# Optimization experiments

Hardware: AMD Instinct MI355X
Metric: run time of the kernel (lower is better)

The kernel has to match this reference:

```python
import jax, jax.numpy as jnp
import numpy as np

HEADS = 20          # 1280 / 64 head_dim, standard SD UNet attention
LORA_SCALE = 1.0    # lora_scale init arg


def setup_inputs() -> dict:
    key = jax.random.key(0)
    ks = jax.random.split(key, 16)
    def w(k, shape, s=0.02):
        return jax.random.normal(k, shape, dtype=jnp.float32) * s
    H, C, R = 1280, 768, 64  # hidden_size, cross_attention_dim, lora_rank
    return {
        "hidden_states": jax.random.normal(ks[0], (16, 4096, H), dtype=jnp.float32),
        "encoder_hidden_states": jax.random.normal(ks[1], (16, 77, C), dtype=jnp.float32),
        # base attention projections (diffusers: q/k/v no bias, to_out has bias)
        "Wq": w(ks[2], (H, H)), "Wk": w(ks[3], (C, H)), "Wv": w(ks[4], (C, H)),
        "Wo": w(ks[5], (H, H)), "bo": jnp.zeros((H,), dtype=jnp.float32),
        # LoRA adapters (down: in->rank, up: rank->out, no bias)
        "q_down": w(ks[6], (H, R)), "q_up": w(ks[7], (R, H)),
        "k_down": w(ks[8], (C, R)), "k_up": w(ks[9], (R, H)),
        "v_down": w(ks[10], (C, R)), "v_up": w(ks[11], (R, H)),
        "o_down": w(ks[12], (H, R)), "o_up": w(ks[13], (R, H)),
    }


def reference(hidden_states, encoder_hidden_states, Wq, Wk, Wv, Wo, bo,
              q_down, q_up, k_down, k_up, v_down, v_up, o_down, o_up):
    b, sq, _ = hidden_states.shape
    # base projections + LoRA low-rank corrections
    q = hidden_states @ Wq + LORA_SCALE * ((hidden_states @ q_down) @ q_up)
    k = encoder_hidden_states @ Wk + LORA_SCALE * ((encoder_hidden_states @ k_down) @ k_up)
    v = encoder_hidden_states @ Wv + LORA_SCALE * ((encoder_hidden_states @ v_down) @ v_up)

    d = q.shape[-1] // HEADS
    def split_heads(x):  # [b, s, h*d] -> [b, h, s, d]
        return x.reshape(x.shape[0], x.shape[1], HEADS, d).transpose(0, 2, 1, 3)
    qh, kh, vh = split_heads(q), split_heads(k), split_heads(v)

    # scaled dot-product attention (no mask, non-causal, dropout=0)
    scale = 1.0 / np.sqrt(d).astype(np.float32)
    scores = jnp.einsum('bhqd,bhkd->bhqk', qh, kh) * scale
    probs = jax.nn.softmax(scores, axis=-1)
    attn_out = jnp.einsum('bhqk,bhkd->bhqd', probs, vh)
    attn_out = attn_out.transpose(0, 2, 1, 3).reshape(b, sq, HEADS * d)

    # output projection + LoRA on W_O
    out = attn_out @ Wo + bo + LORA_SCALE * ((attn_out @ o_down) @ o_up)
    return out
```

## Files before the change

### kernel.cpp

```cpp
#include <hip/hip_runtime.h>
#include <hip/hip_bf16.h>
#include <stdint.h>

typedef unsigned short u16;
typedef __attribute__((ext_vector_type(8))) short short8;
typedef __attribute__((ext_vector_type(4))) float f32x4;

__device__ __forceinline__ u16 f2bf(float f) {
  union { float f; unsigned u; } v; v.f = f;
  unsigned r = v.u + 0x7fffu + ((v.u >> 16) & 1u);
  return (u16)(r >> 16);
}

__device__ __forceinline__ void g2lds16(const u16* g, u16* l) {
  __builtin_amdgcn_global_load_lds(
      (const __attribute__((address_space(1))) uint32_t*)g,
      (__attribute__((address_space(3))) uint32_t*)l, 16, 0, 0);
}

#define BAR()   asm volatile("s_barrier" ::: "memory")
#define LGKM0() asm volatile("s_waitcnt lgkmcnt(0)" ::: "memory")
#define VM8()   asm volatile("s_waitcnt vmcnt(8)" ::: "memory")
#define VM0()   asm volatile("s_waitcnt vmcnt(0)" ::: "memory")
#define PRIO1() __builtin_amdgcn_s_setprio(1)
#define PRIO0() __builtin_amdgcn_s_setprio(0)

#define QSCALE 0.18033688f

__global__ __launch_bounds__(256) void k_convert(const float* __restrict__ in,
                                                 u16* __restrict__ out, int n8) {
  int i = blockIdx.x * 256 + threadIdx.x;
  if (i >= n8) return;
  const float4* p = (const float4*)(in + (size_t)i * 8);
  float4 a = p[0], b = p[1];
  short8 o;
  o[0] = (short)f2bf(a.x); o[1] = (short)f2bf(a.y);
  o[2] = (short)f2bf(a.z); o[3] = (short)f2bf(a.w);
  o[4] = (short)f2bf(b.x); o[5] = (short)f2bf(b.y);
  o[6] = (short)f2bf(b.z); o[7] = (short)f2bf(b.w);
  *(short8*)(out + (size_t)i * 8) = o;
}

__global__ __launch_bounds__(256) void k_prep(
    const float* __restrict__ ehs, u16* __restrict__ ehs_b,
    const float* __restrict__ Wq, const float* __restrict__ qd, const float* __restrict__ qu, u16* __restrict__ wq_t,
    const float* __restrict__ Wk, const float* __restrict__ kd, const float* __restrict__ ku, u16* __restrict__ wk_t,
    const float* __restrict__ Wv, const float* __restrict__ vd, const float* __restrict__ vu, u16* __restrict__ wv_t,
    const float* __restrict__ Wo, const float* __restrict__ od, const float* __restrict__ ou, u16* __restrict__ wo_t) {
  __shared__ float dn[64][65];
  __shared__ float up[64][17];
  int bid = blockIdx.x;

  if (bid < 480) {
    int i = bid * 256 + threadIdx.x;
    short8 o;
    if (i < 118272) {
      const float4* p = (const float4*)(ehs + (size_t)i * 8);
      float4 a = p[0], b = p[1];
      o[0] = (short)f2bf(a.x); o[1] = (short)f2bf(a.y);
      o[2] = (short)f2bf(a.z); o[3] = (short)f2bf(a.w);
      o[4] = (short)f2bf(b.x); o[5] = (short)f2bf(b.y);
      o[6] = (short)f2bf(b.z); o[7] = (short)f2bf(b.w);
    } else {
#pragma unroll
      for (int e = 0; e < 8; ++e) o[e] = 0;
    }
    *(short8*)(ehs_b + (size_t)i * 8) = o;
    return;
  }
  bid -= 480;
  const float *W, *dng, *upg; u16* Wt; int K, bx, by;
  if (bid < 1600)      { W = Wq; dng = qd; upg = qu; Wt = wq_t; K = 1280; bx = bid % 20; by = bid / 20; }
  else if (bid < 2560) { bid -= 1600; W = Wk; dng = kd; upg = ku; Wt = wk_t; K = 768;  bx = bid % 12; by = bid / 12; }
  else if (bid < 3520) { bid -= 2560; W = Wv; dng = vd; upg = vu; Wt = wv_t; K = 768;  bx = bid % 12; by = bid / 12; }
  else                 { bid -= 3520; W = Wo; dng = od; upg = ou; Wt = wo_t; K = 1280; bx = bid % 20; by = bid / 20; }
  const int N = 1280;
  const int k0 = bx * 64, n0 = by * 16;
  const int kc = threadIdx.x & 63, ty = threadIdx.x >> 6;
  for (int c = threadIdx.x; c < 4096; c += 256)
    dn[c >> 6][c & 63] = dng[(size_t)(k0 + (c >> 6)) * 64 + (c & 63)];
  for (int c = threadIdx.x; c < 1024; c += 256)
    up[c >> 4][c & 15] = upg[(size_t)(c >> 4) * N + n0 + (c & 15)];
  __syncthreads();
  float acc[4];
#pragma unroll
  for (int e = 0; e < 4; ++e)
    acc[e] = W[(size_t)(k0 + kc) * N + n0 + ty * 4 + e];
#pragma unroll 16
  for (int r = 0; r < 64; ++r) {
    float d = dn[kc][r];
#pragma unroll
    for (int e = 0; e < 4; ++e) acc[e] += d * up[r][ty * 4 + e];
  }
#pragma unroll
  for (int e = 0; e < 4; ++e)
    Wt[(size_t)(n0 + ty * 4 + e) * K + k0 + kc] = f2bf(acc[e]);
}

__global__ __launch_bounds__(256) void k_gemmKV(const u16* __restrict__ A,
                                                const u16* __restrict__ BtK,
                                                const u16* __restrict__ BtV,
                                                u16* __restrict__ CK,
                                                u16* __restrict__ CV) {
  constexpr int N = 1280, K = 768;
  const u16* Bt = blockIdx.z ? BtV : BtK;
  u16* Cout = blockIdx.z ? CV : CK;
  __shared__ __align__(16) u16 As[128 * 32];
  __shared__ __align__(16) u16 Bs[128 * 32];
  const int tid = threadIdx.x, lane = tid & 63, w = tid >> 6;
  const int n0 = blockIdx.x * 128, m0 = blockIdx.y * 128;
  const int wm = (w >> 1) * 64, wn = (w & 1) * 64;

  f32x4 acc[4][4];
  f32x4 zf = {0.f, 0.f, 0.f, 0.f};
#pragma unroll
  for (int i = 0; i < 4; ++i)
#pragma unroll
    for (int j = 0; j < 4; ++j) acc[i][j] = zf;

  const int c0 = w, c1 = w + 4;
  const int rA0 = c0 * 16 + (lane >> 2), rA1 = c1 * 16 + (lane >> 2);
  const int kp = (lane & 3) * 8;
  const u16* gA0 = A + (size_t)(m0 + rA0) * K + kp;
  const u16* gA1 = A + (size_t)(m0 + rA1) * K + kp;
  const u16* gB0 = Bt + (size_t)(n0 + rA0) * K + kp;
  const u16* gB1 = Bt + (size_t)(n0 + rA1) * K + kp;
  u16* lA0 = As + c0 * 512;  u16* lA1 = As + c1 * 512;
  u16* lB0 = Bs + c0 * 512;  u16* lB1 = Bs + c1 * 512;

  const int fr = lane & 15, kg = (lane >> 4) * 8;

  for (int k0 = 0; k0 < K; k0 += 32) {
    g2lds16(gA0 + k0, lA0);
    g2lds16(gA1 + k0, lA1);
    g2lds16(gB0 + k0, lB0);
    g2lds16(gB1 + k0, lB1);
    __syncthreads();
    short8 af[4], bf[4];
#pragma unroll
    for (int i = 0; i < 4; ++i)
      af[i] = *(const short8*)(As + (wm + i * 16 + fr) * 32 + kg);
#pragma unroll
    for (int j = 0; j < 4; ++j)
      bf[j] = *(const short8*)(Bs + (wn + j * 16 + fr) * 32 + kg);
#pragma unroll
    for (int i = 0; i < 4; ++i)
#pragma unroll
      for (int j = 0; j < 4; ++j)
        acc[i][j] = __builtin_amdgcn_mfma_f32_16x16x32_bf16(af[i], bf[j], acc[i][j], 0, 0, 0);
    __syncthreads();
  }

  const int rb = (lane >> 4) * 4;
#pragma unroll
  for (int i = 0; i < 4; ++i)
#pragma unroll
    for (int j = 0; j < 4; ++j) {
      int col = n0 + wn + j * 16 + fr;
#pragma unroll
      for (int r = 0; r < 4; ++r) {
        int row = m0 + wm + i * 16 + rb + r;
        Cout[(size_t)row * N + col] = f2bf(acc[i][j][r]);
      }
    }
}

#define GEMM256_TILE_RD()                                                      \
  constexpr int K = 1280;                                                      \
  constexpr int N = 1280;                                                      \
  __shared__ __align__(16) u16 lds[2][2][2][128 * 64];                         \
  const int lane = threadIdx.x & 63, w = threadIdx.x >> 6;                     \
  const int bid = blockIdx.x;                                                  \
  const int tile = (bid & 7) * 160 + (bid >> 3);                               \
  const int n0 = (tile % 5) * 256, m0 = (tile / 5) * 256;                      \
  const int l0 = w * 2;                                                        \
  const int fr = lane & 15;                                                    \
  const int q16b = (lane >> 4) * 16;                                           \
  const int xr = (fr & 7) << 4;                                                \
  const int cT0 = ((0 + q16b) ^ xr) >> 1;                                      \
  const int cT1 = ((64 + q16b) ^ xr) >> 1;                                     \
  const int ha = w >> 2;                                                       \
  const int hb = (w & 3) >> 1;                                                 \
  const int rB0 = (w & 1) * 64;

#define LOAD_AF(P, IB)                                                         \
  do {                                                                         \
    _Pragma("unroll") for (int ii = 0; ii < 4; ++ii) {                         \
      const u16* rp = &lds[P][0][ha][(((IB) + ii) * 16 + fr) * 64];            \
      af[ii][0] = *(const short8*)(rp + cT0);                                  \
      af[ii][1] = *(const short8*)(rp + cT1);                                  \
    }                                                                          \
  } while (0)

#define LOAD_BF(P, JB)                                                         \
  do {                                                                         \
    _Pragma("unroll") for (int jj = 0; jj < 2; ++jj) {                         \
      const u16* rp = &lds[P][1][hb][(rB0 + ((JB) + jj) * 16 + fr) * 64];      \
      bf[(JB) + jj][0] = *(const short8*)(rp + cT0);                           \
      bf[(JB) + jj][1] = *(const short8*)(rp + cT1);                           \
    }                                                                          \
  } while (0)

#define MFMA_Q(IO, JB)                                                         \
  do {                                                                         \
    _Pragma("unroll") for (int t = 0; t < 2; ++t)                              \
        _Pragma("unroll") for (int ii = 0; ii < 4; ++ii)                       \
            _Pragma("unroll") for (int jj = 0; jj < 2; ++jj)                   \
                acc[(IO) + ii][(JB) + jj] =                                    \
        __builtin_amdgcn_mfma_f32_16x16x32_bf16(                               \
            af[ii][t], bf[(JB) + jj][t], acc[(IO) + ii][(JB) + jj], 0, 0, 0);  \
  } while (0)

#define ACC_ZERO()                                                             \
  do {                                                                         \
    f32x4 zf = {0.f, 0.f, 0.f, 0.f};                                           \
    _Pragma("unroll") for (int i = 0; i < 8; ++i)                              \
        _Pragma("unroll") for (int j = 0; j < 4; ++j) acc[i][j] = zf;          \
  } while (0)

template <int OUT_MODE>
__global__ __launch_bounds__(512, 2) void k_gemm256f(const u16* __restrict__ A,
                                                     const u16* __restrict__ Bt,
                                                     void* __restrict__ Cout,
                                                     const float* __restrict__ bias) {
  GEMM256_TILE_RD();
  const u16* gsrc[8];
#pragma unroll
  for (int s = 0; s < 8; ++s) {
    const int side = s >> 2, h = (s >> 1) & 1, l = s & 1;
    const int o = (l0 + l) * 1024 + lane * 16;
    const int row = o >> 7;
    const int scol = (o & 127) ^ ((row & 7) << 4);
    const u16* base = side ? (Bt + (size_t)(n0 + h * 128 + row) * K)
                           : (A + (size_t)(m0 + h * 128 + row) * K);
    gsrc[s] = base + (scol >> 1);
  }

#define STAGE(P, KT)                                                           \
  do {                                                                         \
    _Pragma("unroll") for (int s = 0; s < 8; ++s) {                            \
      const int side = s >> 2, h = (s >> 1) & 1, l = s & 1;                    \
      g2lds16(gsrc[s] + (KT) * 64, &lds[P][side][h][(l0 + l) * 512]);          \
    }                                                                          \
  } while (0)

  short8 af[4][2], bf[4][2];
  f32x4 acc[8][4];
  ACC_ZERO();

  STAGE(0, 0);
  STAGE(1, 1);
  VM8();
  BAR();

  for (int t = 0; t < 20; ++t) {
    const int P = t & 1;
    LOAD_AF(P, 0);
    LOAD_BF(P, 0);
    LOAD_BF(P, 2);
    MFMA_Q(0, 0);
    MFMA_Q(0, 2);
    LOAD_AF(P, 4);
    MFMA_Q(4, 2);
    LGKM0();
    BAR();
    if (t < 18) STAGE(P, t + 2);
    PRIO1(); MFMA_Q(4, 0); PRIO0();
    if (t < 18) { VM8(); } else { VM0(); }
    BAR();
  }
#undef STAGE

  const int rb = (lane >> 4) * 4;
  const int orow = m0 + (w >> 2) * 128;
  const int ocol = n0 + (w & 3) * 64;
  if (OUT_MODE == 1) {
    float* C = (float*)Cout;
#pragma unroll
    for (int i = 0; i < 8; ++i)
#pragma unroll
      for (int j = 0; j < 4; ++j) {
        const int col = ocol + j * 16 + fr;
        const float bj = bias[col];
#pragma unroll
        for (int r = 0; r < 4; ++r)
          C[(size_t)(orow + i * 16 + rb + r) * N + col] = acc[i][j][r] + bj;
      }
  } else {
    u16* C = (u16*)Cout;
#pragma unroll
    for (int i = 0; i < 8; ++i)
#pragma unroll
      for (int j = 0; j < 4; ++j) {
        const int col = ocol + j * 16 + fr;
#pragma unroll
        for (int r = 0; r < 4; ++r)
          C[(size_t)(orow + i * 16 + rb + r) * N + col] = f2bf(acc[i][j][r] * QSCALE);
      }
  }
}

__global__ __launch_bounds__(256) void k_attn(u16* __restrict__ Q,
                                              const u16* __restrict__ Kb,
                                              const u16* __restrict__ Vb) {
  const int mt = blockIdx.x, h = blockIdx.y, b = blockIdx.z;
  const int tid = threadIdx.x, lane = tid & 63, w = tid >> 6;
  const int m0 = b * 4096 + mt * 128;
  const int ccol = h * 64;

  __shared__ __align__(16) u16 Qs[128 * 64];
  __shared__ __align__(16) u16 Kl[80 * 72];
  __shared__ __align__(16) u16 Vt[64 * 104];
  __shared__ __align__(16) u16 Pl[128 * 104];

#pragma unroll
  for (int c = 0; c < 4; ++c) {
    const int o = (c * 4 + w) * 1024 + lane * 16;
    const int row = o >> 7;
    const int scol = (o & 127) ^ ((row & 7) << 4);
    g2lds16(Q + (size_t)(m0 + row) * 1280 + ccol + (scol >> 1),
            Qs + (size_t)(c * 4 + w) * 512);
  }

  {
    short8 zz;
#pragma unroll
    for (int e = 0; e < 8; ++e) zz[e] = 0;
    if (tid < 27) ((short8*)Kl)[693 + tid] = zz;
    { const int prow = tid >> 1, pc0 = 80 + (tid & 1) * 8;
      *(short8*)(Pl + prow * 104 + pc0) = zz; }
    for (int c = tid; c < 2048; c += 256)
      Vt[(c >> 5) * 104 + 64 + (c & 31)] = 0;
  }
  for (int c = tid; c < 616; c += 256) {
    int s = c >> 3, d0 = (c & 7) * 8;
    short8 v = *(const short8*)(Kb + (size_t)(b * 77 + s) * 1280 + ccol + d0);
    *(short8*)(Kl + s * 72 + d0) = v;
  }
  for (int c = tid; c < 616; c += 256) {
    int s = c >> 3, d0 = (c & 7) * 8;
    short8 v = *(const short8*)(Vb + (size_t)(b * 77 + s) * 1280 + ccol + d0);
#pragma unroll
    for (int e = 0; e < 8; ++e) Vt[(d0 + e) * 104 + s] = (u16)v[e];
  }
  __syncthreads();

  const int cb = lane & 15;
  const int kq = lane >> 4;
  const int kgu = kq * 8;

  short8 qf[2][2];
#pragma unroll
  for (int i = 0; i < 2; ++i)
#pragma unroll
    for (int t2 = 0; t2 < 2; ++t2) {
      const int r_ = w * 32 + i * 16 + cb;
      const int bc = (t2 * 64 + kq * 16) ^ ((r_ & 7) << 4);
      qf[i][t2] = *(const short8*)(Qs + r_ * 64 + (bc >> 1));
    }

  f32x4 sc[2][5];
  {
    f32x4 zf = {0.f, 0.f, 0.f, 0.f};
#pragma unroll
    for (int i = 0; i < 2; ++i)
#pragma unroll
      for (int j = 0; j < 5; ++j) sc[i][j] = zf;
  }
#pragma unroll
  for (int t2 = 0; t2 < 2; ++t2) {
    short8 kf[5];
#pragma unroll
    for (int j = 0; j < 5; ++j)
      kf[j] = *(const short8*)(Kl + (j * 16 + cb) * 72 + t2 * 32 + kgu);
#pragma unroll
    for (int i = 0; i < 2; ++i)
#pragma unroll
      for (int j = 0; j < 5; ++j)
        sc[i][j] = __builtin_amdgcn_mfma_f32_16x16x32_bf16(qf[i][t2], kf[j], sc[i][j], 0, 0, 0);
  }

  float inv[2][4];
#pragma unroll
  for (int i = 0; i < 2; ++i) {
#pragma unroll
    for (int r = 0; r < 4; ++r) {
      float sum = 0.f;
#pragma unroll
      for (int j = 0; j < 4; ++j) {
        float pv = exp2f(sc[i][j][r]);
        sc[i][j][r] = pv;
        sum += pv;
      }
      {
        float pv = (cb < 13) ? exp2f(sc[i][4][r]) : 0.f;
        sc[i][4][r] = pv;
        sum += pv;
      }
#pragma unroll
      for (int mk = 8; mk >= 1; mk >>= 1) sum += __shfl_xor(sum, mk, 64);
      inv[i][r] = 1.f / sum;
    }
  }

  {
    const int rbase = kq * 4;
#pragma unroll
    for (int i = 0; i < 2; ++i)
#pragma unroll
      for (int j = 0; j < 5; ++j)
#pragma unroll
        for (int r = 0; r < 4; ++r)
          Pl[(w * 32 + i * 16 + rbase + r) * 104 + j * 16 + cb] = f2bf(sc[i][j][r]);
  }
  __syncthreads();

  f32x4 o[2][4];
  {
    f32x4 zf = {0.f, 0.f, 0.f, 0.f};
#pragma unroll
    for (int i = 0; i < 2; ++i)
#pragma unroll
      for (int n = 0; n < 4; ++n) o[i][n] = zf;
  }
#pragma unroll
  for (int t2 = 0; t2 < 3; ++t2) {
    short8 pf[2], vf[4];
#pragma unroll
    for (int i = 0; i < 2; ++i)
      pf[i] = *(const short8*)(Pl + (w * 32 + i * 16 + cb) * 104 + t2 * 32 + kgu);
#pragma unroll
    for (int n = 0; n < 4; ++n)
      vf[n] = *(const short8*)(Vt + (n * 16 + cb) * 104 + t2 * 32 + kgu);
#pragma unroll
    for (int i = 0; i < 2; ++i)
#pragma unroll
      for (int n = 0; n < 4; ++n)
        o[i][n] = __builtin_amdgcn_mfma_f32_16x16x32_bf16(pf[i], vf[n], o[i][n], 0, 0, 0);
  }

  {
    const int rbase = kq * 4;
#pragma unroll
    for (int i = 0; i < 2; ++i)
#pragma unroll
      for (int n = 0; n < 4; ++n)
#pragma unroll
        for (int r = 0; r < 4; ++r)
          Pl[(w * 32 + i * 16 + rbase + r) * 104 + n * 16 + cb] =
              f2bf(o[i][n][r] * inv[i][r]);
  }
  __syncthreads();

#pragma unroll
  for (int c2 = 0; c2 < 4; ++c2) {
    const int o2 = (c2 * 256 + tid) * 16;
    const int row = o2 >> 7, bc = (o2 & 127) >> 1;
    short8 v = *(const short8*)(Pl + row * 104 + bc);
    *(short8*)(Q + (size_t)(m0 + row) * 1280 + ccol + bc) = v;
  }
}

extern "C" void kernel_launch(void* const* d_in, const int* in_sizes, int n_in,
                              void* d_out, int out_size, void* d_ws, size_t ws_size,
                              hipStream_t stream) {
  (void)in_sizes; (void)n_in; (void)out_size; (void)ws_size;
  const float* hs  = (const float*)d_in[0];
  const float* ehs = (const float*)d_in[1];
  const float* Wq  = (const float*)d_in[2];
  const float* Wk  = (const float*)d_in[3];
  const float* Wv  = (const float*)d_in[4];
  const float* Wo  = (const float*)d_in[5];
  const float* bo  = (const float*)d_in[6];
  const float* qd  = (const float*)d_in[7];
  const float* qu  = (const float*)d_in[8];
  const float* kd  = (const float*)d_in[9];
  const float* ku  = (const float*)d_in[10];
  const float* vd  = (const float*)d_in[11];
  const float* vu  = (const float*)d_in[12];
  const float* od  = (const float*)d_in[13];
  const float* ou  = (const float*)d_in[14];

  char* p = (char*)d_ws;
  u16* q_buf = (u16*)p;  p += (size_t)65536 * 1280 * 2;
  u16* wq_t  = (u16*)p;  p += (size_t)1280 * 1280 * 2;
  u16* wo_t  = (u16*)p;  p += (size_t)1280 * 1280 * 2;
  u16* wk_t  = (u16*)p;  p += (size_t)1280 * 768 * 2;
  u16* wv_t  = (u16*)p;  p += (size_t)1280 * 768 * 2;
  u16* ehs_b = (u16*)p;  p += (size_t)1280 * 768 * 2;
  u16* k_buf = (u16*)p;  p += (size_t)1280 * 1280 * 2;
  u16* v_buf = (u16*)p;  p += (size_t)1280 * 1280 * 2;
  u16* hs_b  = (u16*)d_out;

  k_convert<<<40960, 256, 0, stream>>>(hs, hs_b, 10485760);
  k_prep<<<5600, 256, 0, stream>>>(ehs, ehs_b,
                                   Wq, qd, qu, wq_t,
                                   Wk, kd, ku, wk_t,
                                   Wv, vd, vu, wv_t,
                                   Wo, od, ou, wo_t);

  k_gemm256f<2><<<1280, 512, 0, stream>>>(hs_b, wq_t, q_buf, nullptr);
  k_gemmKV<<<dim3(10, 10, 2), 256, 0, stream>>>(ehs_b, wk_t, wv_t, k_buf, v_buf);

  k_attn<<<dim3(32, 20, 16), 256, 0, stream>>>(q_buf, k_buf, v_buf);

  k_gemm256f<1><<<1280, 512, 0, stream>>>(q_buf, wo_t, d_out, bo);
}
```

Measured before the change: 746.7 us.

## Load B operand directly from global to registers in Q-projection GEMM

Adds a GEMM variant that stages only the A tile through LDS and loads the weight (B) fragments straight from global memory into registers each k-step. LDS use per block is halved and B no longer makes an LDS round trip, while the waitcnt thresholds are adjusted to match. Only the Q projection uses the new kernel. The direct global loads of B are less coalesced and sit in the critical path right before the MFMAs, so latency may be exposed.

```diff
diff --git a/kernel.cpp b/kernel.cpp
--- a/kernel.cpp
+++ b/kernel.cpp
@@ -21,6 +21,7 @@
 #define BAR()   asm volatile("s_barrier" ::: "memory")
 #define LGKM0() asm volatile("s_waitcnt lgkmcnt(0)" ::: "memory")
 #define VM8()   asm volatile("s_waitcnt vmcnt(8)" ::: "memory")
+#define VM4()   asm volatile("s_waitcnt vmcnt(4)" ::: "memory")
 #define VM0()   asm volatile("s_waitcnt vmcnt(0)" ::: "memory")
 #define PRIO1() __builtin_amdgcn_s_setprio(1)
 #define PRIO0() __builtin_amdgcn_s_setprio(0)
@@ -165,10 +166,9 @@
     }
 }
 
-#define GEMM256_TILE_RD()                                                      \
+#define GEMM256_COMMON()                                                       \
   constexpr int K = 1280;                                                      \
   constexpr int N = 1280;                                                      \
-  __shared__ __align__(16) u16 lds[2][2][2][128 * 64];                         \
   const int lane = threadIdx.x & 63, w = threadIdx.x >> 6;                     \
   const int bid = blockIdx.x;                                                  \
   const int tile = (bid & 7) * 160 + (bid >> 3);                               \
@@ -183,24 +183,6 @@
   const int hb = (w & 3) >> 1;                                                 \
   const int rB0 = (w & 1) * 64;
 
-#define LOAD_AF(P, IB)                                                         \
-  do {                                                                         \
-    _Pragma("unroll") for (int ii = 0; ii < 4; ++ii) {                         \
-      const u16* rp = &lds[P][0][ha][(((IB) + ii) * 16 + fr) * 64];            \
-      af[ii][0] = *(const short8*)(rp + cT0);                                  \
-      af[ii][1] = *(const short8*)(rp + cT1);                                  \
-    }                                                                          \
-  } while (0)
-
-#define LOAD_BF(P, JB)                                                         \
-  do {                                                                         \
-    _Pragma("unroll") for (int jj = 0; jj < 2; ++jj) {                         \
-      const u16* rp = &lds[P][1][hb][(rB0 + ((JB) + jj) * 16 + fr) * 64];      \
-      bf[(JB) + jj][0] = *(const short8*)(rp + cT0);                           \
-      bf[(JB) + jj][1] = *(const short8*)(rp + cT1);                           \
-    }                                                                          \
-  } while (0)
-
 #define MFMA_Q(IO, JB)                                                         \
   do {                                                                         \
     _Pragma("unroll") for (int t = 0; t < 2; ++t)                              \
@@ -223,7 +205,8 @@
                                                      const u16* __restrict__ Bt,
                                                      void* __restrict__ Cout,
                                                      const float* __restrict__ bias) {
-  GEMM256_TILE_RD();
+  GEMM256_COMMON();
+  __shared__ __align__(16) u16 lds[2][2][2][128 * 64];
   const u16* gsrc[8];
 #pragma unroll
   for (int s = 0; s < 8; ++s) {
@@ -241,6 +224,22 @@
     _Pragma("unroll") for (int s = 0; s < 8; ++s) {                            \
       const int side = s >> 2, h = (s >> 1) & 1, l = s & 1;                    \
       g2lds16(gsrc[s] + (KT) * 64, &lds[P][side][h][(l0 + l) * 512]);          \
+    }                                                                          \
+  } while (0)
+#define LOAD_AF(P, IB)                                                         \
+  do {                                                                         \
+    _Pragma("unroll") for (int ii = 0; ii < 4; ++ii) {                         \
+      const u16* rp = &lds[P][0][ha][(((IB) + ii) * 16 + fr) * 64];            \
+      af[ii][0] = *(const short8*)(rp + cT0);                                  \
+      af[ii][1] = *(const short8*)(rp + cT1);                                  \
+    }                                                                          \
+  } while (0)
+#define LOAD_BF(P, JB)                                                         \
+  do {                                                                         \
+    _Pragma("unroll") for (int jj = 0; jj < 2; ++jj) {                         \
+      const u16* rp = &lds[P][1][hb][(rB0 + ((JB) + jj) * 16 + fr) * 64];      \
+      bf[(JB) + jj][0] = *(const short8*)(rp + cT0);                           \
+      bf[(JB) + jj][1] = *(const short8*)(rp + cT1);                           \
     }                                                                          \
   } while (0)
 
@@ -270,6 +269,107 @@
     BAR();
   }
 #undef STAGE
+#undef LOAD_AF
+#undef LOAD_BF
+
+  const int rb = (lane >> 4) * 4;
+  const int orow = m0 + (w >> 2) * 128;
+  const int ocol = n0 + (w & 3) * 64;
+  if (OUT_MODE == 1) {
+    float* C = (float*)Cout;
+#pragma unroll
+    for (int i = 0; i < 8; ++i)
+#pragma unroll
+      for (int j = 0; j < 4; ++j) {
+        const int col = ocol + j * 16 + fr;
+        const float bj = bias[col];
+#pragma unroll
+        for (int r = 0; r < 4; ++r)
+          C[(size_t)(orow + i * 16 + rb + r) * N + col] = acc[i][j][r] + bj;
+      }
+  } else {
+    u16* C = (u16*)Cout;
+#pragma unroll
+    for (int i = 0; i < 8; ++i)
+#pragma unroll
+      for (int j = 0; j < 4; ++j) {
+        const int col = ocol + j * 16 + fr;
+#pragma unroll
+        for (int r = 0; r < 4; ++r)
+          C[(size_t)(orow + i * 16 + rb + r) * N + col] = f2bf(acc[i][j][r] * QSCALE);
+      }
+  }
+}
+
+template <int OUT_MODE>
+__global__ __launch_bounds__(512, 2) void k_gemm256r(const u16* __restrict__ A,
+                                                     const u16* __restrict__ Bt,
+                                                     void* __restrict__ Cout,
+                                                     const float* __restrict__ bias) {
+  GEMM256_COMMON();
+  __shared__ __align__(16) u16 lds[2][2][128 * 64];
+  const u16* gsrcA[4];
+#pragma unroll
+  for (int s = 0; s < 4; ++s) {
+    const int h = s >> 1, l = s & 1;
+    const int o = (l0 + l) * 1024 + lane * 16;
+    const int row = o >> 7;
+    const int scol = (o & 127) ^ ((row & 7) << 4);
+    gsrcA[s] = A + (size_t)(m0 + h * 128 + row) * K + (scol >> 1);
+  }
+  const u16* gBr[4];
+#pragma unroll
+  for (int j = 0; j < 4; ++j)
+    gBr[j] = Bt + (size_t)(n0 + hb * 128 + rB0 + j * 16 + fr) * K + (lane >> 4) * 8;
+
+#define STAGEA(P, KT)                                                          \
+  do {                                                                         \
+    _Pragma("unroll") for (int s = 0; s < 4; ++s)                              \
+      g2lds16(gsrcA[s] + (KT) * 64, &lds[P][s >> 1][(l0 + (s & 1)) * 512]);    \
+  } while (0)
+#define BLOADQ(KT)                                                             \
+  do {                                                                         \
+    _Pragma("unroll") for (int j = 0; j < 4; ++j)                              \
+        _Pragma("unroll") for (int t2 = 0; t2 < 2; ++t2)                       \
+            bf[j][t2] = *(const short8*)(gBr[j] + (KT) * 64 + t2 * 32);        \
+  } while (0)
+#define LOAD_AFr(P, IB)                                                        \
+  do {                                                                         \
+    _Pragma("unroll") for (int ii = 0; ii < 4; ++ii) {                         \
+      const u16* rp = &lds[P][ha][(((IB) + ii) * 16 + fr) * 64];               \
+      af[ii][0] = *(const short8*)(rp + cT0);                                  \
+      af[ii][1] = *(const short8*)(rp + cT1);                                  \
+    }                                                                          \
+  } while (0)
+
+  short8 af[4][2], bf[4][2];
+  f32x4 acc[8][4];
+  ACC_ZERO();
+
+  STAGEA(0, 0);
+  STAGEA(1, 1);
+  VM4();
+  BAR();
+
+  for (int t = 0; t < 20; ++t) {
+    const int P = t & 1;
+    BLOADQ(t);
+    LOAD_AFr(P, 0);
+    MFMA_Q(0, 0);
+    MFMA_Q(0, 2);
+    LOAD_AFr(P, 4);
+    MFMA_Q(4, 2);
+    LGKM0();
+    BAR();
+    if (t < 18) STAGEA(P, t + 2);
+    PRIO1(); MFMA_Q(4, 0); PRIO0();
+    if (t < 18) { VM4(); }
+    else if (t == 18) { VM0(); }
+    BAR();
+  }
+#undef STAGEA
+#undef BLOADQ
+#undef LOAD_AFr
 
   const int rb = (lane >> 4) * 4;
   const int orow = m0 + (w >> 2) * 128;
@@ -499,7 +599,7 @@
                                    Wv, vd, vu, wv_t,
                                    Wo, od, ou, wo_t);
 
-  k_gemm256f<2><<<1280, 512, 0, stream>>>(hs_b, wq_t, q_buf, nullptr);
+  k_gemm256r<2><<<1280, 512, 0, stream>>>(hs_b, wq_t, q_buf, nullptr);
   k_gemmKV<<<dim3(10, 10, 2), 256, 0, stream>>>(ehs_b, wk_t, wv_t, k_buf, v_buf);
 
   k_attn<<<dim3(32, 20, 16), 256, 0, stream>>>(q_buf, k_buf, v_buf);
```

Result: slower. 882.2 us (+18.1%).

## Fuse hidden-state convert into prep kernel and interleave Q-GEMM staging with MFMA

Applied to the files above, without the earlier changes.

Merges the fp32-to-bf16 conversion of hidden_states into the weight-prep kernel, which saves one launch and lets the small prep blocks overlap with the bulk conversion. Adds a new Q-projection GEMM variant that unrolls two k-steps per iteration. It splits global-to-LDS staging into half-tile chunks spread between MFMA quarter-groups, with barriers and priority bumps around each MFMA group, so memory issue is spread more evenly across the compute. The extra barriers add synchronisation overhead, and the finer vmcnt accounting (VM6/VM8) must match the order of issued loads.

```diff
diff --git a/kernel.cpp b/kernel.cpp
--- a/kernel.cpp
+++ b/kernel.cpp
@@ -21,27 +21,15 @@
 #define BAR()   asm volatile("s_barrier" ::: "memory")
 #define LGKM0() asm volatile("s_waitcnt lgkmcnt(0)" ::: "memory")
 #define VM8()   asm volatile("s_waitcnt vmcnt(8)" ::: "memory")
+#define VM6()   asm volatile("s_waitcnt vmcnt(6)" ::: "memory")
 #define VM0()   asm volatile("s_waitcnt vmcnt(0)" ::: "memory")
 #define PRIO1() __builtin_amdgcn_s_setprio(1)
 #define PRIO0() __builtin_amdgcn_s_setprio(0)
 
 #define QSCALE 0.18033688f
 
-__global__ __launch_bounds__(256) void k_convert(const float* __restrict__ in,
-                                                 u16* __restrict__ out, int n8) {
-  int i = blockIdx.x * 256 + threadIdx.x;
-  if (i >= n8) return;
-  const float4* p = (const float4*)(in + (size_t)i * 8);
-  float4 a = p[0], b = p[1];
-  short8 o;
-  o[0] = (short)f2bf(a.x); o[1] = (short)f2bf(a.y);
-  o[2] = (short)f2bf(a.z); o[3] = (short)f2bf(a.w);
-  o[4] = (short)f2bf(b.x); o[5] = (short)f2bf(b.y);
-  o[6] = (short)f2bf(b.z); o[7] = (short)f2bf(b.w);
-  *(short8*)(out + (size_t)i * 8) = o;
-}
-
-__global__ __launch_bounds__(256) void k_prep(
+__global__ __launch_bounds__(256) void k_prepc(
+    const float* __restrict__ hs, u16* __restrict__ hs_b,
     const float* __restrict__ ehs, u16* __restrict__ ehs_b,
     const float* __restrict__ Wq, const float* __restrict__ qd, const float* __restrict__ qu, u16* __restrict__ wq_t,
     const float* __restrict__ Wk, const float* __restrict__ kd, const float* __restrict__ ku, u16* __restrict__ wk_t,
@@ -51,6 +39,19 @@
   __shared__ float up[64][17];
   int bid = blockIdx.x;
 
+  if (bid < 40960) {
+    int i = bid * 256 + threadIdx.x;
+    const float4* p = (const float4*)(hs + (size_t)i * 8);
+    float4 a = p[0], b = p[1];
+    short8 o;
+    o[0] = (short)f2bf(a.x); o[1] = (short)f2bf(a.y);
+    o[2] = (short)f2bf(a.z); o[3] = (short)f2bf(a.w);
+    o[4] = (short)f2bf(b.x); o[5] = (short)f2bf(b.y);
+    o[6] = (short)f2bf(b.z); o[7] = (short)f2bf(b.w);
+    *(short8*)(hs_b + (size_t)i * 8) = o;
+    return;
+  }
+  bid -= 40960;
   if (bid < 480) {
     int i = bid * 256 + threadIdx.x;
     short8 o;
@@ -165,7 +166,7 @@
     }
 }
 
-#define GEMM256_TILE_RD()                                                      \
+#define GEMM256_COMMON()                                                       \
   constexpr int K = 1280;                                                      \
   constexpr int N = 1280;                                                      \
   __shared__ __align__(16) u16 lds[2][2][2][128 * 64];                         \
@@ -183,6 +184,34 @@
   const int hb = (w & 3) >> 1;                                                 \
   const int rB0 = (w & 1) * 64;
 
+#define GSRC_INIT(A_, Bt_)                                                     \
+  const u16* gsrc[4][2];                                                       \
+  _Pragma("unroll") for (int s2 = 0; s2 < 4; ++s2) {                           \
+    const int side = s2 >> 1, h = s2 & 1;                                      \
+    _Pragma("unroll") for (int l = 0; l < 2; ++l) {                            \
+      const int o = (l0 + l) * 1024 + lane * 16;                               \
+      const int row = o >> 7;                                                  \
+      const int scol = (o & 127) ^ ((row & 7) << 4);                           \
+      const u16* base = side ? ((Bt_) + (size_t)(n0 + h * 128 + row) * K)      \
+                             : ((A_) + (size_t)(m0 + h * 128 + row) * K);      \
+      gsrc[s2][l] = base + (scol >> 1);                                        \
+    }                                                                          \
+  }
+
+#define STAGE_HALF(P, SIDE, H, KT)                                             \
+  do {                                                                         \
+    g2lds16(gsrc[(SIDE) * 2 + (H)][0] + (KT) * 64,                             \
+            &lds[P][SIDE][H][(l0 + 0) * 512]);                                 \
+    g2lds16(gsrc[(SIDE) * 2 + (H)][1] + (KT) * 64,                             \
+            &lds[P][SIDE][H][(l0 + 1) * 512]);                                 \
+  } while (0)
+
+#define STAGE_FULL(P, KT)                                                      \
+  do {                                                                         \
+    STAGE_HALF(P, 0, 0, KT); STAGE_HALF(P, 0, 1, KT);                          \
+    STAGE_HALF(P, 1, 0, KT); STAGE_HALF(P, 1, 1, KT);                          \
+  } while (0)
+
 #define LOAD_AF(P, IB)                                                         \
   do {                                                                         \
     _Pragma("unroll") for (int ii = 0; ii < 4; ++ii) {                         \
@@ -218,38 +247,44 @@
         _Pragma("unroll") for (int j = 0; j < 4; ++j) acc[i][j] = zf;          \
   } while (0)
 
+#define GEMM256_EPI_F32BIAS()                                                  \
+  do {                                                                         \
+    float* C = (float*)Cout;                                                   \
+    _Pragma("unroll") for (int i = 0; i < 8; ++i)                              \
+        _Pragma("unroll") for (int j = 0; j < 4; ++j) {                        \
+      const int col = ocol + j * 16 + fr;                                      \
+      const float bj = bias[col];                                              \
+      _Pragma("unroll") for (int r = 0; r < 4; ++r)                            \
+          C[(size_t)(orow + i * 16 + rb + r) * N + col] = acc[i][j][r] + bj;   \
+    }                                                                          \
+  } while (0)
+
+#define GEMM256_EPI_BF16SCALE()                                                \
+  do {                                                                         \
+    u16* C = (u16*)Cout;                                                       \
+    _Pragma("unroll") for (int i = 0; i < 8; ++i)                              \
+        _Pragma("unroll") for (int j = 0; j < 4; ++j) {                        \
+      const int col = ocol + j * 16 + fr;                                      \
+      _Pragma("unroll") for (int r = 0; r < 4; ++r)                            \
+          C[(size_t)(orow + i * 16 + rb + r) * N + col] =                      \
+              f2bf(acc[i][j][r] * QSCALE);                                     \
+    }                                                                          \
+  } while (0)
+
 template <int OUT_MODE>
 __global__ __launch_bounds__(512, 2) void k_gemm256f(const u16* __restrict__ A,
                                                      const u16* __restrict__ Bt,
                                                      void* __restrict__ Cout,
                                                      const float* __restrict__ bias) {
-  GEMM256_TILE_RD();
-  const u16* gsrc[8];
-#pragma unroll
-  for (int s = 0; s < 8; ++s) {
-    const int side = s >> 2, h = (s >> 1) & 1, l = s & 1;
-    const int o = (l0 + l) * 1024 + lane * 16;
-    const int row = o >> 7;
-    const int scol = (o & 127) ^ ((row & 7) << 4);
-    const u16* base = side ? (Bt + (size_t)(n0 + h * 128 + row) * K)
-                           : (A + (size_t)(m0 + h * 128 + row) * K);
-    gsrc[s] = base + (scol >> 1);
-  }
-
-#define STAGE(P, KT)                                                           \
-  do {                                                                         \
-    _Pragma("unroll") for (int s = 0; s < 8; ++s) {                            \
-      const int side = s >> 2, h = (s >> 1) & 1, l = s & 1;                    \
-      g2lds16(gsrc[s] + (KT) * 64, &lds[P][side][h][(l0 + l) * 512]);          \
-    }                                                                          \
-  } while (0)
+  GEMM256_COMMON();
+  GSRC_INIT(A, Bt);
 
   short8 af[4][2], bf[4][2];
   f32x4 acc[8][4];
   ACC_ZERO();
 
-  STAGE(0, 0);
-  STAGE(1, 1);
+  STAGE_FULL(0, 0);
+  STAGE_FULL(1, 1);
   VM8();
   BAR();
 
@@ -264,40 +299,66 @@
     MFMA_Q(4, 2);
     LGKM0();
     BAR();
-    if (t < 18) STAGE(P, t + 2);
+    if (t < 18) STAGE_FULL(P, t + 2);
     PRIO1(); MFMA_Q(4, 0); PRIO0();
     if (t < 18) { VM8(); } else { VM0(); }
     BAR();
   }
-#undef STAGE
 
   const int rb = (lane >> 4) * 4;
   const int orow = m0 + (w >> 2) * 128;
   const int ocol = n0 + (w & 3) * 64;
-  if (OUT_MODE == 1) {
-    float* C = (float*)Cout;
-#pragma unroll
-    for (int i = 0; i < 8; ++i)
-#pragma unroll
-      for (int j = 0; j < 4; ++j) {
-        const int col = ocol + j * 16 + fr;
-        const float bj = bias[col];
-#pragma unroll
-        for (int r = 0; r < 4; ++r)
-          C[(size_t)(orow + i * 16 + rb + r) * N + col] = acc[i][j][r] + bj;
-      }
-  } else {
-    u16* C = (u16*)Cout;
-#pragma unroll
-    for (int i = 0; i < 8; ++i)
-#pragma unroll
-      for (int j = 0; j < 4; ++j) {
-        const int col = ocol + j * 16 + fr;
-#pragma unroll
-        for (int r = 0; r < 4; ++r)
-          C[(size_t)(orow + i * 16 + rb + r) * N + col] = f2bf(acc[i][j][r] * QSCALE);
-      }
-  }
+  if (OUT_MODE == 1) { GEMM256_EPI_F32BIAS(); }
+  else               { GEMM256_EPI_BF16SCALE(); }
+}
+
+__global__ __launch_bounds__(512, 2) void k_gemm256p(const u16* __restrict__ A,
+                                                     const u16* __restrict__ Bt,
+                                                     void* __restrict__ Cout) {
+  GEMM256_COMMON();
+  GSRC_INIT(A, Bt);
+
+  short8 af[4][2], bf[4][2];
+  f32x4 acc[8][4];
+  ACC_ZERO();
+
+  STAGE_FULL(0, 0);
+  STAGE_FULL(1, 1);
+  VM8();
+  BAR();
+
+  for (int it = 0; it < 10; ++it) {
+    const bool st = (it < 9);
+    const int t2 = 2 * it + 2, t3 = 2 * it + 3;
+    LOAD_AF(0, 0); LOAD_BF(0, 0);
+    BAR(); LGKM0(); PRIO1(); MFMA_Q(0, 0); PRIO0(); BAR();
+    LOAD_BF(0, 2);
+    BAR(); LGKM0(); PRIO1(); MFMA_Q(0, 2); PRIO0(); BAR();
+    LOAD_AF(0, 4);
+    if (st) STAGE_HALF(0, 1, 0, t2);
+    BAR(); LGKM0(); PRIO1(); MFMA_Q(4, 2); PRIO0(); BAR();
+    if (st) { STAGE_HALF(0, 1, 1, t2); STAGE_HALF(0, 0, 0, t2); }
+    PRIO1(); MFMA_Q(4, 0); PRIO0();
+    if (st) { VM6(); } else { VM0(); }
+    BAR();
+    LOAD_AF(1, 0); LOAD_BF(1, 0);
+    if (st) STAGE_HALF(0, 0, 1, t2);
+    BAR(); LGKM0(); PRIO1(); MFMA_Q(0, 0); PRIO0(); BAR();
+    LOAD_BF(1, 2);
+    BAR(); LGKM0(); PRIO1(); MFMA_Q(0, 2); PRIO0(); BAR();
+    LOAD_AF(1, 4);
+    if (st) STAGE_HALF(1, 1, 0, t3);
+    BAR(); LGKM0(); PRIO1(); MFMA_Q(4, 2); PRIO0(); BAR();
+    if (st) { STAGE_HALF(1, 1, 1, t3); STAGE_HALF(1, 0, 0, t3); STAGE_HALF(1, 0, 1, t3); }
+    PRIO1(); MFMA_Q(4, 0); PRIO0();
+    if (st) { VM8(); } else { VM0(); }
+    BAR();
+  }
+
+  const int rb = (lane >> 4) * 4;
+  const int orow = m0 + (w >> 2) * 128;
+  const int ocol = n0 + (w & 3) * 64;
+  GEMM256_EPI_BF16SCALE();
 }
 
 __global__ __launch_bounds__(256) void k_attn(u16* __restrict__ Q,
@@ -492,14 +553,13 @@
   u16* v_buf = (u16*)p;  p += (size_t)1280 * 1280 * 2;
   u16* hs_b  = (u16*)d_out;
 
-  k_convert<<<40960, 256, 0, stream>>>(hs, hs_b, 10485760);
-  k_prep<<<5600, 256, 0, stream>>>(ehs, ehs_b,
-                                   Wq, qd, qu, wq_t,
-                                   Wk, kd, ku, wk_t,
-                                   Wv, vd, vu, wv_t,
-                                   Wo, od, ou, wo_t);
-
-  k_gemm256f<2><<<1280, 512, 0, stream>>>(hs_b, wq_t, q_buf, nullptr);
+  k_prepc<<<46560, 256, 0, stream>>>(hs, hs_b, ehs, ehs_b,
+                                     Wq, qd, qu, wq_t,
+                                     Wk, kd, ku, wk_t,
+                                     Wv, vd, vu, wv_t,
+                                     Wo, od, ou, wo_t);
+
+  k_gemm256p<<<1280, 512, 0, stream>>>(hs_b, wq_t, q_buf);
   k_gemmKV<<<dim3(10, 10, 2), 256, 0, stream>>>(ehs_b, wk_t, wv_t, k_buf, v_buf);
 
   k_attn<<<dim3(32, 20, 16), 256, 0, stream>>>(q_buf, k_buf, v_buf);
```

After: 726.1 us. 1.03x faster.
